# Performance work log

Measured on AMD Instinct MI355X. Metric: run time of the kernel, lower is better.

## Reference

```python
import jax, jax.numpy as jnp
import numpy as np


def _gcn_conv(x, W, b, src, dst, deg_inv_sqrt, n_nodes):
    # x: [N, Fin], W: [Fin, Fout]; edges (with self-loops): src, dst [E+N]
    h = x @ W  # [N, Fout]
    norm = deg_inv_sqrt[src] * deg_inv_sqrt[dst]  # [E+N]
    msgs = h[src] * norm[:, None]  # gather-multiply
    out = jax.ops.segment_sum(msgs, dst, num_segments=n_nodes)  # scatter-add
    return out + b


def setup_inputs() -> dict:
    key = jax.random.key(0)
    k1, k2, k3, k4 = jax.random.split(key, 4)
    N, E, FIN, HID, OUT = 100000, 3200000, 128, 32, 32
    x = jax.random.normal(k1, (N, FIN), dtype=jnp.float32)
    edge_index = jax.random.randint(k2, (2, E), 0, N, dtype=jnp.int64)
    W1 = jax.random.normal(k3, (FIN, HID), dtype=jnp.float32) * (1.0 / np.sqrt(FIN))
    b1 = jnp.zeros((HID,), dtype=jnp.float32)
    W2 = jax.random.normal(k4, (HID, OUT), dtype=jnp.float32) * (1.0 / np.sqrt(HID))
    b2 = jnp.zeros((OUT,), dtype=jnp.float32)
    return {"x": x, "edge_index": edge_index, "W1": W1, "b1": b1, "W2": W2, "b2": b2}


def reference(x, edge_index, W1, b1, W2, b2):
    n = x.shape[0]
    # GCNConv defaults: add self-loops, symmetric normalization D^-1/2 (A+I) D^-1/2
    loops = jnp.arange(n, dtype=edge_index.dtype)
    src = jnp.concatenate([edge_index[0], loops])
    dst = jnp.concatenate([edge_index[1], loops])
    deg = jax.ops.segment_sum(jnp.ones_like(dst, dtype=x.dtype), dst, num_segments=n)
    deg_inv_sqrt = jnp.where(deg > 0, jax.lax.rsqrt(jnp.maximum(deg, 1.0)), 0.0)
    h = jax.nn.relu(_gcn_conv(x, W1, b1, src, dst, deg_inv_sqrt, n))  # hidden layer + ReLU
    out = jax.nn.relu(_gcn_conv(h, W2, b2, src, dst, deg_inv_sqrt, n))  # last layer + last_activation relu
    return out
```

## Files before the change

kernel.cpp:

```cpp
#include <hip/hip_runtime.h>
#include <hip/hip_fp16.h>

#define FIN 128
#define HID 32
#define BSHIFT 8
#define BNODES 256
#define CHUNK 2048
#define NBMAX 512
#define CAPB 8960


__global__ __launch_bounds__(256) void chunk_sort_kernel(const int* __restrict__ src,
                                                         const int* __restrict__ dst,
                                                         int* __restrict__ ec,
                                                         unsigned short* __restrict__ offt,
                                                         int E, int nb) {
    __shared__ int hist[NBMAX];
    __shared__ int pref[NBMAX];
    __shared__ int wsum[128];
    __shared__ int sorted[CHUNK];
    int c = blockIdx.x, t = threadIdx.x;
    int beg = c * CHUNK;
    int cnt = min(CHUNK, E - beg);
    for (int i = t; i < nb; i += 256) hist[i] = 0;
    __syncthreads();
    int bk[8], ent[8];
    #pragma unroll
    for (int j = 0; j < 8; ++j) {
        int i = t + j * 256;
        if (i < cnt) {
            int d = dst[beg + i];
            bk[j]  = ((unsigned)d) >> BSHIFT;
            ent[j] = src[beg + i] | ((d & (BNODES - 1)) << 24);
            atomicAdd(&hist[bk[j]], 1);
        } else bk[j] = -1;
    }
    __syncthreads();
    if (t < 128) {
        int s = 0;
        #pragma unroll
        for (int j = 0; j < 4; ++j) {
            int idx = t * 4 + j;
            int v = (idx < nb) ? hist[idx] : 0;
            pref[idx] = s; s += v;
        }
        wsum[t] = s;
    }
    __syncthreads();
    if (t == 0) { int run = 0; for (int j = 0; j < 128; ++j) { int v = wsum[j]; wsum[j] = run; run += v; } }
    __syncthreads();
    for (int i = t; i < nb; i += 256) { int p = pref[i] + wsum[i >> 2]; pref[i] = p; hist[i] = p; }
    __syncthreads();
    #pragma unroll
    for (int j = 0; j < 8; ++j) {
        if (bk[j] >= 0) {
            int p = atomicAdd(&hist[bk[j]], 1);
            sorted[p] = ent[j];
        }
    }
    __syncthreads();
    for (int i = t; i < cnt; i += 256) ec[(size_t)c * CHUNK + i] = sorted[i];
    unsigned short* row = offt + (size_t)c * (nb + 1);
    for (int i = t; i < nb; i += 256) row[i] = (unsigned short)pref[i];
    if (t == 0) row[nb] = (unsigned short)cnt;
}


__global__ __launch_bounds__(1024) void bucket_build_kernel(const int* __restrict__ ec,
                                                            const unsigned short* __restrict__ offt,
                                                            int* __restrict__ entries,
                                                            float* __restrict__ dinv,
                                                            int* __restrict__ rowbeg,
                                                            int* __restrict__ rowcnt,
                                                            int n, int nb, int nchunks, int cap) {
    __shared__ int raw[CAPB];
    __shared__ int srt[CAPB];
    __shared__ int hist[BNODES];
    __shared__ int pref[BNODES];
    __shared__ int cursor[BNODES];
    __shared__ int wsum[64];
    __shared__ int nfill;
    int b = blockIdx.x, t = threadIdx.x;
    if (t < BNODES) hist[t] = 0;
    if (t == 0) nfill = 0;
    __syncthreads();
    for (int c = t; c < nchunks; c += 1024) {
        const unsigned short* row = offt + (size_t)c * (nb + 1);
        int s = row[b], e2 = row[b + 1];
        int m = e2 - s;
        if (m > 0) {
            int base = atomicAdd(&nfill, m);
            const int* p = ec + (size_t)c * CHUNK + s;
            for (int k = 0; k < m; ++k) {
                int e = p[k];
                if (base + k < CAPB) raw[base + k] = e;
                atomicAdd(&hist[((unsigned)e) >> 24], 1);
            }
        }
    }
    __syncthreads();
    int total = min(nfill, CAPB);
    if (t < 64) {
        int s = 0;
        #pragma unroll
        for (int j = 0; j < 4; ++j) { int v = hist[t * 4 + j]; pref[t * 4 + j] = s; s += v; }
        wsum[t] = s;
    }
    __syncthreads();
    if (t == 0) { int run = 0; for (int j = 0; j < 64; ++j) { int v = wsum[j]; wsum[j] = run; run += v; } }
    __syncthreads();
    if (t < BNODES) { int p = pref[t] + wsum[t >> 2]; pref[t] = p; cursor[t] = p; }
    __syncthreads();
    for (int i = t; i < total; i += 1024) {
        int e = raw[i];
        int p = atomicAdd(&cursor[((unsigned)e) >> 24], 1);
        srt[p] = e;
    }
    __syncthreads();
    int* ep = entries + (size_t)b * cap;
    for (int i = t; i < total; i += 1024) ep[i] = srt[i];
    int node = b * BNODES + t;
    if (t < BNODES && node < n) {
        int deg = hist[t];
        dinv[node]   = rsqrtf((float)deg + 1.0f);
        rowbeg[node] = b * cap + pref[t];
        rowcnt[node] = deg;
    }
}


__global__ __launch_bounds__(256) void gemm1_kernel(const float* __restrict__ x,
                                                    const float* __restrict__ W,
                                                    const float* __restrict__ dinv,
                                                    __half* __restrict__ h16, int n) {
    __shared__ float Ws[FIN * HID];
    __shared__ float xs[8][FIN];
    int t = threadIdx.x;
    for (int i = t; i < FIN * HID; i += 256) Ws[i] = W[i];
    int row0 = blockIdx.x * 8;
    {
        int r  = t >> 5;
        int c4 = (t & 31) * 4;
        int row = row0 + r;
        float4 v = (row < n) ? *(const float4*)&x[(size_t)row * FIN + c4]
                             : make_float4(0.f, 0.f, 0.f, 0.f);
        *(float4*)&xs[r][c4] = v;
    }
    __syncthreads();
    int r = t >> 5, col = t & 31;
    int row = row0 + r;
    if (row < n) {
        float acc = 0.f;
        #pragma unroll 16
        for (int k = 0; k < FIN; ++k) acc += xs[r][k] * Ws[k * HID + col];
        h16[(size_t)row * HID + col] = __float2half(acc * dinv[row]);
    } else {
        h16[(size_t)row * HID + col] = __float2half(0.f);
    }
}


__global__ __launch_bounds__(256) void gather_kernel(const int* __restrict__ entries,
                                                     const int* __restrict__ rowbeg,
                                                     const int* __restrict__ rowcnt,
                                                     const float* __restrict__ dinv,
                                                     const __half* __restrict__ h16,
                                                     const float* __restrict__ bias,
                                                     float* __restrict__ out, int n, int sent) {
    int g = threadIdx.x >> 5, f = threadIdx.x & 31;
    int i = blockIdx.x * 8 + g;
    if (i >= n) return;
    float di = dinv[i];
    float s = __half2float(h16[(size_t)i * HID + f]);
    int beg = rowbeg[i], cnt = rowcnt[i];
    for (int base = 0; base < cnt; base += 32) {
        int idx = beg + base + f;
        int sv = ((base + f) < cnt) ? entries[idx] : sent;
        float hv[32];
        #pragma unroll
        for (int j = 0; j < 32; ++j) {
            int e = __shfl(sv, j, 32);
            hv[j] = __half2float(h16[(size_t)(e & 0xFFFFFF) * HID + f]);
        }
        #pragma unroll
        for (int j = 0; j < 32; ++j) s += hv[j];
    }
    float r = bias[f] + di * s;
    out[(size_t)i * HID + f] = fmaxf(r, 0.f);
}


__global__ __launch_bounds__(256) void gemm2_kernel(const float* __restrict__ hin,
                                                    const float* __restrict__ W,
                                                    const float* __restrict__ dinv,
                                                    __half* __restrict__ h16, int n) {
    __shared__ float Ws[HID * HID];
    __shared__ float hs[8][HID];
    int t = threadIdx.x;
    for (int i = t; i < HID * HID; i += 256) Ws[i] = W[i];
    int row0 = blockIdx.x * 8;
    {
        int r = t >> 5, c = t & 31;
        int row = row0 + r;
        hs[r][c] = (row < n) ? hin[(size_t)row * HID + c] : 0.f;
    }
    __syncthreads();
    int r = t >> 5, col = t & 31;
    int row = row0 + r;
    if (row < n) {
        float s = 0.f;
        #pragma unroll
        for (int k = 0; k < HID; ++k) s += hs[r][k] * Ws[k * HID + col];
        h16[(size_t)row * HID + col] = __float2half(s * dinv[row]);
    } else {
        h16[(size_t)row * HID + col] = __float2half(0.f);
    }
}

extern "C" void kernel_launch(void* const* d_in, const int* in_sizes, int n_in,
                              void* d_out, int out_size, void* d_ws, size_t ws_size,
                              hipStream_t stream) {
    const float* x  = (const float*)d_in[0];
    const int*   ei = (const int*)d_in[1];
    const float* W1 = (const float*)d_in[2];
    const float* b1 = (const float*)d_in[3];
    const float* W2 = (const float*)d_in[4];
    const float* b2 = (const float*)d_in[5];
    float* out = (float*)d_out;

    int n = in_sizes[0] / FIN;
    int E = in_sizes[1] / 2;
    const int* src = ei;
    const int* dst = ei + E;

    int nb = (n + BNODES - 1) / BNODES;
    int nchunks = (E + CHUNK - 1) / CHUNK;
    int ngrid = (n + 8) / 8;
    int npad = ngrid * 8;
    int cap = CAPB;

    char* ws = (char*)d_ws;
    size_t off = 0;
    auto alloc = [&](size_t bytes) { char* p = ws + off; off += (bytes + 255) & ~(size_t)255; return p; };
    int*            ec      = (int*)alloc((size_t)nchunks * CHUNK * 4);
    unsigned short* offt    = (unsigned short*)alloc((size_t)nchunks * (nb + 1) * 2);
    int*            entries = (int*)alloc((size_t)nb * cap * 4);
    float*          dinv    = (float*)alloc((size_t)n * 4);
    int*            rowbeg  = (int*)alloc((size_t)n * 4);
    int*            rowcnt  = (int*)alloc((size_t)n * 4);
    float*          acc     = (float*)alloc((size_t)n * HID * 4);
    __half*         hh      = (__half*)alloc((size_t)npad * HID * 2);

    chunk_sort_kernel<<<nchunks, 256, 0, stream>>>(src, dst, ec, offt, E, nb);
    bucket_build_kernel<<<nb, 1024, 0, stream>>>(ec, offt, entries, dinv, rowbeg, rowcnt,
                                                 n, nb, nchunks, cap);

    gemm1_kernel<<<ngrid, 256, 0, stream>>>(x, W1, dinv, hh, n);
    gather_kernel<<<(n + 7) / 8, 256, 0, stream>>>(entries, rowbeg, rowcnt, dinv, hh, b1, acc, n, n);

    gemm2_kernel<<<ngrid, 256, 0, stream>>>(acc, W2, dinv, hh, n);
    gather_kernel<<<(n + 7) / 8, 256, 0, stream>>>(entries, rowbeg, rowcnt, dinv, hh, b2, out, n, n);
}
```

Measured before the change: 281.0 us.

## Register-tile gemm1 with 64-row blocks and 2x4 outputs per thread

Rewrites the first-layer GEMM so each block loads 64 rows of x into padded shared memory and each thread computes a 2-row by 4-column output tile with float4 shared loads. The W1 shared-memory load is amortized over eight times more rows, and per-FMA shared memory traffic drops because of register reuse. The cost is more shared memory per block (about 50KB), which may reduce occupancy. gemm2 keeps its old grid, and the padded h16 buffer is sized to the new row granularity.

```diff
diff --git a/kernel.cpp b/kernel.cpp
--- a/kernel.cpp
+++ b/kernel.cpp
@@ -8,6 +8,8 @@
 #define CHUNK 2048
 #define NBMAX 512
 #define CAPB 8960
+#define G1ROWS 64
+#define XPAD 4
 
 
 __global__ __launch_bounds__(256) void chunk_sort_kernel(const int* __restrict__ src,
@@ -134,28 +136,59 @@
                                                     const float* __restrict__ dinv,
                                                     __half* __restrict__ h16, int n) {
     __shared__ float Ws[FIN * HID];
-    __shared__ float xs[8][FIN];
+    __shared__ float xs[G1ROWS][FIN + XPAD];
     int t = threadIdx.x;
     for (int i = t; i < FIN * HID; i += 256) Ws[i] = W[i];
-    int row0 = blockIdx.x * 8;
-    {
-        int r  = t >> 5;
-        int c4 = (t & 31) * 4;
+    int row0 = blockIdx.x * G1ROWS;
+    for (int idx = t; idx < G1ROWS * (FIN / 4); idx += 256) {
+        int r  = idx >> 5;
+        int c4 = (idx & 31) * 4;
         int row = row0 + r;
         float4 v = (row < n) ? *(const float4*)&x[(size_t)row * FIN + c4]
                              : make_float4(0.f, 0.f, 0.f, 0.f);
         *(float4*)&xs[r][c4] = v;
     }
     __syncthreads();
-    int r = t >> 5, col = t & 31;
-    int row = row0 + r;
-    if (row < n) {
-        float acc = 0.f;
-        #pragma unroll 16
-        for (int k = 0; k < FIN; ++k) acc += xs[r][k] * Ws[k * HID + col];
-        h16[(size_t)row * HID + col] = __float2half(acc * dinv[row]);
-    } else {
-        h16[(size_t)row * HID + col] = __float2half(0.f);
+    int tr = t >> 3, tc = t & 7;
+    int r0 = tr * 2, c0 = tc * 4;
+    float4 a0 = make_float4(0.f, 0.f, 0.f, 0.f);
+    float4 a1 = make_float4(0.f, 0.f, 0.f, 0.f);
+    #pragma unroll 8
+    for (int k4 = 0; k4 < FIN / 4; ++k4) {
+        float4 xv0 = *(const float4*)&xs[r0][k4 * 4];
+        float4 xv1 = *(const float4*)&xs[r0 + 1][k4 * 4];
+        float4 w0 = *(const float4*)&Ws[(k4 * 4 + 0) * HID + c0];
+        float4 w1 = *(const float4*)&Ws[(k4 * 4 + 1) * HID + c0];
+        float4 w2 = *(const float4*)&Ws[(k4 * 4 + 2) * HID + c0];
+        float4 w3 = *(const float4*)&Ws[(k4 * 4 + 3) * HID + c0];
+        a0.x = fmaf(xv0.x, w0.x, a0.x); a0.y = fmaf(xv0.x, w0.y, a0.y);
+        a0.z = fmaf(xv0.x, w0.z, a0.z); a0.w = fmaf(xv0.x, w0.w, a0.w);
+        a0.x = fmaf(xv0.y, w1.x, a0.x); a0.y = fmaf(xv0.y, w1.y, a0.y);
+        a0.z = fmaf(xv0.y, w1.z, a0.z); a0.w = fmaf(xv0.y, w1.w, a0.w);
+        a0.x = fmaf(xv0.z, w2.x, a0.x); a0.y = fmaf(xv0.z, w2.y, a0.y);
+        a0.z = fmaf(xv0.z, w2.z, a0.z); a0.w = fmaf(xv0.z, w2.w, a0.w);
+        a0.x = fmaf(xv0.w, w3.x, a0.x); a0.y = fmaf(xv0.w, w3.y, a0.y);
+        a0.z = fmaf(xv0.w, w3.z, a0.z); a0.w = fmaf(xv0.w, w3.w, a0.w);
+        a1.x = fmaf(xv1.x, w0.x, a1.x); a1.y = fmaf(xv1.x, w0.y, a1.y);
+        a1.z = fmaf(xv1.x, w0.z, a1.z); a1.w = fmaf(xv1.x, w0.w, a1.w);
+        a1.x = fmaf(xv1.y, w1.x, a1.x); a1.y = fmaf(xv1.y, w1.y, a1.y);
+        a1.z = fmaf(xv1.y, w1.z, a1.z); a1.w = fmaf(xv1.y, w1.w, a1.w);
+        a1.x = fmaf(xv1.z, w2.x, a1.x); a1.y = fmaf(xv1.z, w2.y, a1.y);
+        a1.z = fmaf(xv1.z, w2.z, a1.z); a1.w = fmaf(xv1.z, w2.w, a1.w);
+        a1.x = fmaf(xv1.w, w3.x, a1.x); a1.y = fmaf(xv1.w, w3.y, a1.y);
+        a1.z = fmaf(xv1.w, w3.z, a1.z); a1.w = fmaf(xv1.w, w3.w, a1.w);
+    }
+    #pragma unroll
+    for (int rr = 0; rr < 2; ++rr) {
+        int row = row0 + r0 + rr;
+        float4 a = rr ? a1 : a0;
+        float di = (row < n) ? dinv[row] : 0.f;
+        float sc = (row < n) ? di : 0.f;
+        __half2 p0 = __floats2half2_rn(a.x * sc, a.y * sc);
+        __half2 p1 = __floats2half2_rn(a.z * sc, a.w * sc);
+        __half2* dst = (__half2*)&h16[(size_t)row * HID + c0];
+        dst[0] = p0;
+        dst[1] = p1;
     }
 }
 
@@ -235,8 +268,8 @@
 
     int nb = (n + BNODES - 1) / BNODES;
     int nchunks = (E + CHUNK - 1) / CHUNK;
-    int ngrid = (n + 8) / 8;
-    int npad = ngrid * 8;
+    int g1grid = (n + G1ROWS) / G1ROWS;
+    int npad = g1grid * G1ROWS;
     int cap = CAPB;
 
     char* ws = (char*)d_ws;
@@ -255,9 +288,9 @@
     bucket_build_kernel<<<nb, 1024, 0, stream>>>(ec, offt, entries, dinv, rowbeg, rowcnt,
                                                  n, nb, nchunks, cap);
 
-    gemm1_kernel<<<ngrid, 256, 0, stream>>>(x, W1, dinv, hh, n);
+    gemm1_kernel<<<g1grid, 256, 0, stream>>>(x, W1, dinv, hh, n);
     gather_kernel<<<(n + 7) / 8, 256, 0, stream>>>(entries, rowbeg, rowcnt, dinv, hh, b1, acc, n, n);
 
-    gemm2_kernel<<<ngrid, 256, 0, stream>>>(acc, W2, dinv, hh, n);
+    gemm2_kernel<<<(n + 8) / 8, 256, 0, stream>>>(acc, W2, dinv, hh, n);
     gather_kernel<<<(n + 7) / 8, 256, 0, stream>>>(entries, rowbeg, rowcnt, dinv, hh, b2, out, n, n);
 }
```

Result: faster. 267.3 us (-4.9%).
